# Kernel optimization log

Hardware: AMD Instinct MI355X
Metric: run time of the kernel (lower is better)

## Reference

```python
import jax, jax.numpy as jnp
import numpy as np
from jax import lax

HEADS = 4
DIM = 64
GATE_HID = 16


def setup_inputs() -> dict:
    key = jax.random.key(0)
    ks = jax.random.split(key, 12)
    b, c, h, w = 2, DIM, 48, 48
    s = 0.05
    x = jax.random.normal(ks[0], (b, c, h, w), jnp.float32)
    Wqkv = jax.random.normal(ks[1], (3 * c, c), jnp.float32) * s
    bqkv = jax.random.normal(ks[2], (3 * c,), jnp.float32) * s
    Wpos = jax.random.normal(ks[3], (3 * c, 1, 3, 3), jnp.float32) * s
    bpos = jax.random.normal(ks[4], (3 * c,), jnp.float32) * s
    Wg1 = jax.random.normal(ks[5], (GATE_HID, 1), jnp.float32) * 0.5
    bg1 = jax.random.normal(ks[6], (GATE_HID,), jnp.float32) * 0.1
    Wg2 = jax.random.normal(ks[7], (1, GATE_HID), jnp.float32) * 0.5
    bg2 = jax.random.normal(ks[8], (1,), jnp.float32) * 0.1
    Wproj = jax.random.normal(ks[9], (c, c), jnp.float32) * s
    bproj = jax.random.normal(ks[10], (c,), jnp.float32) * s
    return {"x": x, "Wqkv": Wqkv, "bqkv": bqkv, "Wpos": Wpos, "bpos": bpos,
            "Wg1": Wg1, "bg1": bg1, "Wg2": Wg2, "bg2": bg2,
            "Wproj": Wproj, "bproj": bproj}


def _forward(x, Wqkv, bqkv, Wpos, bpos, Wg1, bg1, Wg2, bg2, Wproj, bproj):
    b, c, h, w = x.shape
    n = h * w
    heads = HEADS
    hd = c // heads
    scale = hd ** -0.5
    # qkv 1x1 conv then 3x3 depthwise positional conv
    qkv = jnp.einsum('bchw,oc->bohw', x, Wqkv) + bqkv[None, :, None, None]
    qkv = lax.conv_general_dilated(
        qkv, Wpos, window_strides=(1, 1), padding='SAME',
        feature_group_count=3 * c,
        dimension_numbers=('NCHW', 'OIHW', 'NCHW')) + bpos[None, :, None, None]
    q, k, v = jnp.split(qkv, 3, axis=1)

    def to_heads(t):
        # [b,c,h,w] -> [b,heads,n,hd]
        return t.reshape(b, c, n).transpose(0, 2, 1).reshape(b, n, heads, hd).transpose(0, 2, 1, 3)

    q, k, v = to_heads(q), to_heads(k), to_heads(v)
    attn = jnp.einsum('bhid,bhjd->bhij', q, k) * scale  # [b,heads,n,n]
    prob = jax.nn.softmax(attn, axis=-1)
    entropy = -(prob * jnp.log(jnp.clip(prob, 1e-12))).sum(-1).mean(-1)  # [b,heads]
    # entropy gate: sigmoid(fc2(relu(fc1(e)))) * 0.9 + 0.1
    hgate = jax.nn.relu(entropy[..., None] @ Wg1.T + bg1)  # [b,heads,16]
    ratio = jax.nn.sigmoid(hgate @ Wg2.T + bg2)[..., 0] * 0.9 + 0.1  # [b,heads]
    # dynamic per-(batch,head) top-k along rows via rank threshold
    keep = jnp.clip(jnp.ceil(ratio * n).astype(jnp.int32), 1, n)  # [b,heads]
    sorted_desc = -jnp.sort(-attn, axis=-1)  # [b,heads,n,n]
    idx = jnp.broadcast_to((keep - 1)[:, :, None, None], (b, heads, n, 1))
    thresh = jnp.take_along_axis(sorted_desc, idx, axis=-1)  # [b,heads,n,1]
    sparse = jnp.where(attn >= thresh, attn, -jnp.inf)
    p = jax.nn.softmax(sparse, axis=-1)
    out = jnp.einsum('bhij,bhjd->bhid', p, v)  # [b,heads,n,hd]
    out = out.transpose(0, 2, 1, 3).reshape(b, n, c)
    out = out @ Wproj.T + bproj
    return out.transpose(0, 2, 1).reshape(b, c, h, w)


def reference(x, Wqkv, bqkv, Wpos, bpos, Wg1, bg1, Wg2, bg2, Wproj, bproj):
    return _forward(x, Wqkv, bqkv, Wpos, bpos, Wg1, bg1, Wg2, bg2, Wproj, bproj)
```

## Files before the change

kernel.cpp:

```cpp
#include <hip/hip_runtime.h>
#include <hip/hip_fp16.h>


#define NEG_INF (-__builtin_huge_valf())

typedef _Float16 half8_t __attribute__((ext_vector_type(8)));
typedef float floatx4 __attribute__((ext_vector_type(4)));

__device__ __forceinline__ unsigned h2key(unsigned short u) {
  return (u & 0x8000u) ? (unsigned)((~u) & 0xFFFFu) : (unsigned)(u | 0x8000u);
}
__device__ __forceinline__ float key16_to_float(unsigned k) {
  unsigned short u = (k & 0x8000u) ? (unsigned short)(k & 0x7FFFu)
                                   : (unsigned short)((~k) & 0xFFFFu);
  return __half2float(__ushort_as_half(u));
}

__device__ __forceinline__ void unpack8(uint4 v, float* o) {
  float2 f0 = __half22float2(*(__half2*)&v.x);
  float2 f1 = __half22float2(*(__half2*)&v.y);
  float2 f2 = __half22float2(*(__half2*)&v.z);
  float2 f3 = __half22float2(*(__half2*)&v.w);
  o[0] = f0.x; o[1] = f0.y; o[2] = f1.x; o[3] = f1.y;
  o[4] = f2.x; o[5] = f2.y; o[6] = f3.x; o[7] = f3.y;
}

__global__ __launch_bounds__(256) void k_dw(const float* __restrict__ x,
                                            const float* __restrict__ Wqkv,
                                            const float* __restrict__ bqkv,
                                            const float* __restrict__ Wpos,
                                            const float* __restrict__ bpos,
                                            _Float16* __restrict__ q2,
                                            _Float16* __restrict__ k2,
                                            _Float16* __restrict__ vt,
                                            float* __restrict__ ent) {
  __shared__ float smem[16][384];
  if (blockIdx.x == 0 && threadIdx.x < 8) ent[threadIdx.x] = 0.f;
  int blk = blockIdx.x;
  int chunk = blk % 9;
  int sel = (blk / 9) % 3;
  int head = (blk / 27) % 4;
  int b = blk / 108;
  int chbase = sel * 64 + head * 16;
  int bh = b * 4 + head;
  int tid = threadIdx.x;
  int p0 = chunk * 256;
  int baserow = p0 / 48;
  int rA = min(max(baserow - 1, 0), 40);

  for (int rep = 0; rep < 2; rep++) {
    int pw = tid + rep * 256;
    if (pw < 384) {
      int gpos = rA * 48 + pw;
      const float* xb = x + b * 64 * 2304 + gpos;
      float acc[16];
#pragma unroll
      for (int d = 0; d < 16; d++) acc[d] = bqkv[chbase + d];
#pragma unroll 8
      for (int c = 0; c < 64; c++) {
        float xv = xb[c * 2304];
#pragma unroll
        for (int d = 0; d < 16; d++)
          acc[d] = fmaf(Wqkv[(chbase + d) * 64 + c], xv, acc[d]);
      }
#pragma unroll
      for (int d = 0; d < 16; d++) smem[d][pw] = acc[d];
    }
  }
  __syncthreads();

  int pos = p0 + tid;
  int yy = pos / 48, xx = pos - yy * 48;
  int ry = yy - rA;
  float accv[16];
#pragma unroll
  for (int d = 0; d < 16; d++) {
    const float* w = Wpos + (chbase + d) * 9;
    float a = bpos[chbase + d];
#pragma unroll
    for (int dy = -1; dy <= 1; dy++) {
      int y2 = yy + dy;
      if ((unsigned)y2 < 48u) {
#pragma unroll
        for (int dx = -1; dx <= 1; dx++) {
          int x2 = xx + dx;
          if ((unsigned)x2 < 48u)
            a = fmaf(w[(dy + 1) * 3 + (dx + 1)], smem[d][(ry + dy) * 48 + x2],
                     a);
        }
      }
    }
    accv[d] = a;
  }

  if (sel == 2) {
#pragma unroll
    for (int d = 0; d < 16; d++)
      vt[((size_t)bh * 16 + d) * 2304 + pos] = (_Float16)accv[d];
  } else {
    _Float16 h1[16], h2[16];
#pragma unroll
    for (int d = 0; d < 16; d++) {
      float a = (sel == 0) ? accv[d] * 0.25f : accv[d];
      h1[d] = (_Float16)a;
      h2[d] = (_Float16)(a - (float)h1[d]);
    }
    _Float16* dst = ((sel == 0) ? q2 : k2) + ((size_t)bh * 2304 + pos) * 32;
    uint4* d4 = (uint4*)dst;
    d4[0] = *(uint4*)&h1[0];
    d4[1] = *(uint4*)&h1[8];
    d4[2] = *(uint4*)&h2[0];
    d4[3] = *(uint4*)&h2[8];
  }
}

template <bool STORE>
__global__ __launch_bounds__(256) void k_ent_t(const _Float16* __restrict__ q2,
                                               const _Float16* __restrict__ k2,
                                               float* __restrict__ ent,
                                               _Float16* __restrict__ lgH) {
  __shared__ __align__(16) _Float16 tBuf[4][16][72];
  __shared__ float mWv[4][16];
  __shared__ float mFin[16];
  __shared__ float sWv[4][16], uWv[4][16];

  int blk = blockIdx.x;
  int rowtile = blk % 144;
  int bh = blk / 144;
  int row0 = rowtile * 16;
  int tid = threadIdx.x, lane = tid & 63, wave = tid >> 6;
  int m16 = lane & 15, quad = lane >> 4;

  const half8_t* q2v =
      (const half8_t*)(q2 + ((size_t)bh * 2304 + row0 + m16) * 32);
  half8_t A1 = q2v[quad];
  half8_t zh = {};
  half8_t A2 = (lane < 32) ? A1 : zh;
  const half8_t* kbase = (const half8_t*)(k2 + (size_t)bh * 2304 * 32);

  float mreg[4] = {NEG_INF, NEG_INF, NEG_INF, NEG_INF};
  for (int g = 0; g < 9; g++) {
#pragma unroll
    for (int tt = 0; tt < 4; tt++) {
      int t = g * 4 + tt;
      int col = wave * 576 + t * 16 + m16;
      const half8_t* kk = kbase + (size_t)col * 4;
      half8_t b1 = kk[quad & 1];
      half8_t b2 = kk[2 + (quad & 1)];
      floatx4 acc = {};
      acc = __builtin_amdgcn_mfma_f32_16x16x32_f16(A2, b2, acc, 0, 0, 0);
      acc = __builtin_amdgcn_mfma_f32_16x16x32_f16(A1, b1, acc, 0, 0, 0);
#pragma unroll
      for (int i = 0; i < 4; i++) {
        mreg[i] = fmaxf(mreg[i], acc[i]);
        if (STORE) tBuf[wave][quad * 4 + i][tt * 16 + m16] = (_Float16)acc[i];
      }
    }
    if (STORE) {
      __syncthreads();
      int rb = lane >> 3, seg = lane & 7;
#pragma unroll
      for (int it = 0; it < 2; it++) {
        int rr = it * 8 + rb;
        uint4 vv = *(const uint4*)&tBuf[wave][rr][seg * 8];
        *(uint4*)(lgH + ((size_t)bh * 2304 + row0 + rr) * 2304 + wave * 576 +
                  g * 64 + seg * 8) = vv;
      }
      __syncthreads();
    }
  }
#pragma unroll
  for (int off = 1; off < 16; off <<= 1)
#pragma unroll
    for (int i = 0; i < 4; i++)
      mreg[i] = fmaxf(mreg[i], __shfl_xor(mreg[i], off));
  if (m16 == 0) {
#pragma unroll
    for (int i = 0; i < 4; i++) mWv[wave][quad * 4 + i] = mreg[i];
  }
  __syncthreads();
  if (tid < 16) {
    mFin[tid] = fmaxf(fmaxf(mWv[0][tid], mWv[1][tid]),
                      fmaxf(mWv[2][tid], mWv[3][tid]));
  }
  __syncthreads();

  float mrow[4];
#pragma unroll
  for (int i = 0; i < 4; i++) mrow[i] = mFin[quad * 4 + i];
  float s[4] = {0.f, 0.f, 0.f, 0.f}, u[4] = {0.f, 0.f, 0.f, 0.f};
#pragma unroll 4
  for (int t = 0; t < 36; t++) {
    int col = wave * 576 + t * 16 + m16;
    const half8_t* kk = kbase + (size_t)col * 4;
    half8_t b1 = kk[quad & 1];
    half8_t b2 = kk[2 + (quad & 1)];
    floatx4 acc = {};
    acc = __builtin_amdgcn_mfma_f32_16x16x32_f16(A2, b2, acc, 0, 0, 0);
    acc = __builtin_amdgcn_mfma_f32_16x16x32_f16(A1, b1, acc, 0, 0, 0);
#pragma unroll
    for (int i = 0; i < 4; i++) {
      float z = acc[i] - mrow[i];
      float e = __expf(z);
      s[i] += e;
      u[i] = fmaf(z, e, u[i]);
    }
  }
#pragma unroll
  for (int off = 1; off < 16; off <<= 1) {
#pragma unroll
    for (int i = 0; i < 4; i++) {
      s[i] += __shfl_xor(s[i], off);
      u[i] += __shfl_xor(u[i], off);
    }
  }
  if (m16 == 0) {
#pragma unroll
    for (int i = 0; i < 4; i++) {
      sWv[wave][quad * 4 + i] = s[i];
      uWv[wave][quad * 4 + i] = u[i];
    }
  }
  __syncthreads();
  if (tid < 16) {
    float S = sWv[0][tid] + sWv[1][tid] + sWv[2][tid] + sWv[3][tid];
    float U = uWv[0][tid] + uWv[1][tid] + uWv[2][tid] + uWv[3][tid];
    float er = __logf(S) - U / S;
    er += __shfl_xor(er, 1);
    er += __shfl_xor(er, 2);
    er += __shfl_xor(er, 4);
    er += __shfl_xor(er, 8);
    if (tid == 0) atomicAdd(&ent[bh], er);
  }
}

template <bool CACHED>
__global__ __launch_bounds__(256, 7) void k_attn_t(
    const _Float16* __restrict__ q2, const _Float16* __restrict__ k2,
    const _Float16* __restrict__ vt, const _Float16* __restrict__ lgH,
    const float* __restrict__ ent, const float* __restrict__ Wg1,
    const float* __restrict__ bg1, const float* __restrict__ Wg2,
    const float* __restrict__ bg2, float* __restrict__ oh) {
  __shared__ __align__(16) _Float16 pbuf[4][2320];
  __shared__ float sS[4];
  __shared__ float mShF[4][4];
  __shared__ __align__(16) float redSh[4][64];

  int a = blockIdx.x;
  int v8 = a & 7;
  int idx = a >> 3;
  int q = idx & 3;
  int pi = idx >> 2;
  int bh = pi / 18;
  int rowtile = v8 + (pi % 18) * 8;
  int rowblk = rowtile * 4 + q;
  int row0 = rowblk * 4;
  int tid = threadIdx.x, lane = tid & 63, wave = tid >> 6;

  float eAvg = ent[bh] * (1.f / 2304.f);
  float gacc = bg2[0];
#pragma unroll
  for (int i = 0; i < 16; i++) {
    float h = fmaxf(fmaf(eAvg, Wg1[i], bg1[i]), 0.f);
    gacc = fmaf(h, Wg2[i], gacc);
  }
  float ratio = 0.9f / (1.f + __expf(-gacc)) + 0.1f;
  int kp = (int)ceilf(ratio * 2304.f);
  unsigned keep = (unsigned)min(max(kp, 1), 2304);

  float v[36];
  float m;
  if (CACHED) {
    const _Float16* src = lgH + ((size_t)bh * 2304 + row0 + wave) * 2304;
    const uint4* s4 = (const uint4*)src;
    float mx = NEG_INF;
#pragma unroll
    for (int it = 0; it < 4; it++) {
      uint4 r = s4[lane + it * 64];
      unpack8(r, &v[it * 8]);
    }
    {
      uint2 r2 = *(const uint2*)(src + 2048 + lane * 4);
      float2 f0 = __half22float2(*(__half2*)&r2.x);
      float2 f1 = __half22float2(*(__half2*)&r2.y);
      v[32] = f0.x; v[33] = f0.y; v[34] = f1.x; v[35] = f1.y;
    }
#pragma unroll
    for (int i = 0; i < 36; i++) mx = fmaxf(mx, v[i]);
#pragma unroll
    for (int off = 1; off < 64; off <<= 1) mx = fmaxf(mx, __shfl_xor(mx, off));
    m = mx;
  } else {
    int m16 = lane & 15, quad = lane >> 4;
    const half8_t* q2v =
        (const half8_t*)(q2 + ((size_t)bh * 2304 + row0 + (m16 & 3)) * 32);
    half8_t A1 = q2v[quad];
    half8_t zh = {};
    half8_t A2 = (lane < 32) ? A1 : zh;
    const half8_t* kbase = (const half8_t*)(k2 + (size_t)bh * 2304 * 32);
    float ml[4] = {NEG_INF, NEG_INF, NEG_INF, NEG_INF};
#pragma unroll 4
    for (int t = 0; t < 36; t++) {
      int ct = wave * 36 + t;
      int col = ct * 16 + m16;
      const half8_t* kk = kbase + (size_t)col * 4;
      half8_t b1 = kk[quad & 1];
      half8_t b2 = kk[2 + (quad & 1)];
      floatx4 acc = {};
      acc = __builtin_amdgcn_mfma_f32_16x16x32_f16(A2, b2, acc, 0, 0, 0);
      acc = __builtin_amdgcn_mfma_f32_16x16x32_f16(A1, b1, acc, 0, 0, 0);
      if (lane < 16) {
#pragma unroll
        for (int i = 0; i < 4; i++) {
          pbuf[i][ct * 16 + lane] = (_Float16)acc[i];
          ml[i] = fmaxf(ml[i], acc[i]);
        }
      }
    }
#pragma unroll
    for (int off = 1; off < 16; off <<= 1)
#pragma unroll
      for (int i = 0; i < 4; i++) ml[i] = fmaxf(ml[i], __shfl_xor(ml[i], off));
    if (lane == 0) {
#pragma unroll
      for (int i = 0; i < 4; i++) mShF[wave][i] = ml[i];
    }
    __syncthreads();
    m = fmaxf(fmaxf(mShF[0][wave], mShF[1][wave]),
              fmaxf(mShF[2][wave], mShF[3][wave]));
    const _Float16* src = pbuf[wave];
    const uint4* s4 = (const uint4*)src;
#pragma unroll
    for (int it = 0; it < 4; it++) unpack8(s4[lane + it * 64], &v[it * 8]);
    uint2 r2 = *(const uint2*)(src + 2048 + lane * 4);
    float2 f0 = __half22float2(*(__half2*)&r2.x);
    float2 f1 = __half22float2(*(__half2*)&r2.y);
    v[32] = f0.x; v[33] = f0.y; v[34] = f1.x; v[35] = f1.y;
  }

  float th;
  {
    unsigned T = 0u;
    for (int bit = 15; bit >= 0; --bit) {
      unsigned cand = T | (1u << bit);
      float cf = key16_to_float(cand);
      unsigned cnt = 0u;
#pragma unroll
      for (int i = 0; i < 36; i++)
        cnt += (unsigned)__popcll(__ballot(v[i] >= cf));
      if (cnt >= keep) {
        T = cand;
        if (cnt == keep) break;
      }
    }
    th = key16_to_float(T);
  }

  {
    float sp = 0.f;
    uint4* prow4 = (uint4*)pbuf[wave];
#pragma unroll
    for (int it = 0; it < 4; it++) {
      float p[8];
#pragma unroll
      for (int e = 0; e < 8; e++) {
        float av = v[it * 8 + e];
        p[e] = (av >= th) ? __expf(av - m) : 0.f;
        sp += p[e];
      }
      uint4 o;
      __half2 h0 = __floats2half2_rn(p[0], p[1]); o.x = *(unsigned*)&h0;
      __half2 h1 = __floats2half2_rn(p[2], p[3]); o.y = *(unsigned*)&h1;
      __half2 h2 = __floats2half2_rn(p[4], p[5]); o.z = *(unsigned*)&h2;
      __half2 h3 = __floats2half2_rn(p[6], p[7]); o.w = *(unsigned*)&h3;
      prow4[lane + it * 64] = o;
    }
    {
      float p0 = (v[32] >= th) ? __expf(v[32] - m) : 0.f;
      float p1 = (v[33] >= th) ? __expf(v[33] - m) : 0.f;
      float p2 = (v[34] >= th) ? __expf(v[34] - m) : 0.f;
      float p3 = (v[35] >= th) ? __expf(v[35] - m) : 0.f;
      sp += (p0 + p1) + (p2 + p3);
      uint2 o;
      __half2 h0 = __floats2half2_rn(p0, p1); o.x = *(unsigned*)&h0;
      __half2 h1 = __floats2half2_rn(p2, p3); o.y = *(unsigned*)&h1;
      *(uint2*)(pbuf[wave] + 2048 + lane * 4) = o;
    }
#pragma unroll
    for (int off = 1; off < 64; off <<= 1) sp += __shfl_xor(sp, off);
    if (lane == 0) sS[wave] = sp;
  }
  __syncthreads();

  {
    int m16 = lane & 15, quad = lane >> 4;
    const _Float16* vrow = vt + ((size_t)bh * 16 + m16) * 2304;
    const _Float16* prow = pbuf[m16 & 3];
    int jb0 = wave * 576 + quad * 8;
    floatx4 acc = {};
#pragma unroll 6
    for (int t = 0; t < 18; t++) {
      int jb = jb0 + t * 32;
      half8_t a2 = *(const half8_t*)&prow[jb];
      half8_t b2 = *(const half8_t*)&vrow[jb];
      acc = __builtin_amdgcn_mfma_f32_16x16x32_f16(a2, b2, acc, 0, 0, 0);
    }
    if (lane < 16) {
      *(floatx4*)&redSh[wave][m16 * 4] = acc;
    }
  }
  __syncthreads();
  if (tid < 64) {
    int r = tid & 3, d = tid >> 2;
    float s2 = redSh[0][d * 4 + r] + redSh[1][d * 4 + r] +
               redSh[2][d * 4 + r] + redSh[3][d * 4 + r];
    oh[((size_t)(bh * 2304 + row0 + r)) * 16 + d] = s2 / sS[r];
  }
}

__global__ __launch_bounds__(256) void k_proj(const float* __restrict__ oh,
                                              const float* __restrict__ Wp,
                                              const float* __restrict__ bp,
                                              float* __restrict__ out) {
  int blk = blockIdx.x;
  int chunk = blk % 9;
  int cog = (blk / 9) % 16;
  int b = blk / (9 * 16);
  int co0 = cog * 4;
  int pos = chunk * 256 + threadIdx.x;
  float a0 = bp[co0 + 0], a1 = bp[co0 + 1], a2 = bp[co0 + 2], a3 = bp[co0 + 3];
#pragma unroll
  for (int head = 0; head < 4; head++) {
    const float4* op =
        (const float4*)(oh + ((size_t)((b * 4 + head) * 2304 + pos)) * 16);
#pragma unroll
    for (int p = 0; p < 4; p++) {
      float4 o4 = op[p];
#pragma unroll
      for (int i = 0; i < 4; i++) {
        const float* wr = Wp + (co0 + i) * 64 + head * 16 + p * 4;
        float* ai = (i == 0) ? &a0 : ((i == 1) ? &a1 : ((i == 2) ? &a2 : &a3));
        *ai = fmaf(wr[0], o4.x, *ai);
        *ai = fmaf(wr[1], o4.y, *ai);
        *ai = fmaf(wr[2], o4.z, *ai);
        *ai = fmaf(wr[3], o4.w, *ai);
      }
    }
  }
  out[(b * 64 + co0 + 0) * 2304 + pos] = a0;
  out[(b * 64 + co0 + 1) * 2304 + pos] = a1;
  out[(b * 64 + co0 + 2) * 2304 + pos] = a2;
  out[(b * 64 + co0 + 3) * 2304 + pos] = a3;
}

extern "C" void kernel_launch(void* const* d_in, const int* in_sizes, int n_in,
                              void* d_out, int out_size, void* d_ws,
                              size_t ws_size, hipStream_t stream) {
  const float* x    = (const float*)d_in[0];
  const float* Wqkv = (const float*)d_in[1];
  const float* bqkv = (const float*)d_in[2];
  const float* Wpos = (const float*)d_in[3];
  const float* bpos = (const float*)d_in[4];
  const float* Wg1  = (const float*)d_in[5];
  const float* bg1  = (const float*)d_in[6];
  const float* Wg2  = (const float*)d_in[7];
  const float* bg2  = (const float*)d_in[8];
  const float* Wpr  = (const float*)d_in[9];
  const float* bpr  = (const float*)d_in[10];
  float* out = (float*)d_out;

  const size_t lgBytes = (size_t)8 * 2304 * 2304 * 2;
  const size_t baseBytes =
      (size_t)(294912 + 8) * 4 + (size_t)(2 * 589824 + 294912) * 2;
  bool cached = ws_size >= lgBytes + baseBytes;

  char* base = (char*)d_ws;
  _Float16* lgH = nullptr;
  if (cached) {
    lgH = (_Float16*)base;
    base += lgBytes;
  }
  float* oh = (float*)base;
  float* ent = oh + 294912;
  _Float16* q2 = (_Float16*)(ent + 8);
  _Float16* k2 = q2 + 589824;
  _Float16* vt = k2 + 589824;

  hipLaunchKernelGGL(k_dw, dim3(216), dim3(256), 0, stream,
                     x, Wqkv, bqkv, Wpos, bpos, q2, k2, vt, ent);
  if (cached) {
    hipLaunchKernelGGL((k_ent_t<true>), dim3(8 * 144), dim3(256), 0, stream,
                       q2, k2, ent, lgH);
    hipLaunchKernelGGL((k_attn_t<true>), dim3(8 * 576), dim3(256), 0, stream,
                       q2, k2, vt, lgH, ent, Wg1, bg1, Wg2, bg2, oh);
  } else {
    hipLaunchKernelGGL((k_ent_t<false>), dim3(8 * 144), dim3(256), 0, stream,
                       q2, k2, ent, lgH);
    hipLaunchKernelGGL((k_attn_t<false>), dim3(8 * 576), dim3(256), 0, stream,
                       q2, k2, vt, lgH, ent, Wg1, bg1, Wg2, bg2, oh);
  }
  hipLaunchKernelGGL(k_proj, dim3(2 * 16 * 9), dim3(256), 0, stream,
                     oh, Wpr, bpr, out);
}
```

Before: 218.3 us.

## Split QKV 1x1 conv into its own high-parallelism kernel before depthwise conv

Moves the 1x1 QKV projection out of the depthwise-conv kernel into a separate kernel launched on 864 blocks, each computing 4 output channels for 256 positions, and writes fp32 results to a new workspace buffer. The depthwise kernel then loads its halo tile from that buffer instead of recomputing the projection for 384 halo positions per block. This removes redundant halo recomputation and the low-occupancy 216-block projection, at the cost of an extra launch and a round trip of about 3.5 MB through global memory. The workspace requirement grows, which may change whether the cached-logits path is enabled.

```diff
diff --git a/kernel.cpp b/kernel.cpp
--- a/kernel.cpp
+++ b/kernel.cpp
@@ -7,9 +7,6 @@
 typedef _Float16 half8_t __attribute__((ext_vector_type(8)));
 typedef float floatx4 __attribute__((ext_vector_type(4)));
 
-__device__ __forceinline__ unsigned h2key(unsigned short u) {
-  return (u & 0x8000u) ? (unsigned)((~u) & 0xFFFFu) : (unsigned)(u | 0x8000u);
-}
 __device__ __forceinline__ float key16_to_float(unsigned k) {
   unsigned short u = (k & 0x8000u) ? (unsigned short)(k & 0x7FFFu)
                                    : (unsigned short)((~k) & 0xFFFFu);
@@ -25,17 +22,46 @@
   o[4] = f2.x; o[5] = f2.y; o[6] = f3.x; o[7] = f3.y;
 }
 
-__global__ __launch_bounds__(256) void k_dw(const float* __restrict__ x,
-                                            const float* __restrict__ Wqkv,
-                                            const float* __restrict__ bqkv,
+__global__ __launch_bounds__(256) void k_qkv(const float* __restrict__ x,
+                                             const float* __restrict__ W,
+                                             const float* __restrict__ bias,
+                                             float* __restrict__ out,
+                                             float* __restrict__ ent) {
+  if (blockIdx.x == 0 && threadIdx.x < 8) ent[threadIdx.x] = 0.f;
+  int blk = blockIdx.x;
+  int chunk = blk % 9;
+  int og = (blk / 9) % 48;
+  int b = blk / (9 * 48);
+  int o0 = og * 4;
+  int pos = chunk * 256 + threadIdx.x;
+  const float* xb = x + b * 64 * 2304 + pos;
+  const float* w0 = W + (o0 + 0) * 64;
+  const float* w1 = W + (o0 + 1) * 64;
+  const float* w2 = W + (o0 + 2) * 64;
+  const float* w3 = W + (o0 + 3) * 64;
+  float a0 = bias[o0 + 0], a1 = bias[o0 + 1];
+  float a2 = bias[o0 + 2], a3 = bias[o0 + 3];
+#pragma unroll
+  for (int c = 0; c < 64; c++) {
+    float xv = xb[c * 2304];
+    a0 = fmaf(w0[c], xv, a0);
+    a1 = fmaf(w1[c], xv, a1);
+    a2 = fmaf(w2[c], xv, a2);
+    a3 = fmaf(w3[c], xv, a3);
+  }
+  out[(b * 192 + o0 + 0) * 2304 + pos] = a0;
+  out[(b * 192 + o0 + 1) * 2304 + pos] = a1;
+  out[(b * 192 + o0 + 2) * 2304 + pos] = a2;
+  out[(b * 192 + o0 + 3) * 2304 + pos] = a3;
+}
+
+__global__ __launch_bounds__(256) void k_dw(const float* __restrict__ qkv,
                                             const float* __restrict__ Wpos,
                                             const float* __restrict__ bpos,
                                             _Float16* __restrict__ q2,
                                             _Float16* __restrict__ k2,
-                                            _Float16* __restrict__ vt,
-                                            float* __restrict__ ent) {
+                                            _Float16* __restrict__ vt) {
   __shared__ float smem[16][384];
-  if (blockIdx.x == 0 && threadIdx.x < 8) ent[threadIdx.x] = 0.f;
   int blk = blockIdx.x;
   int chunk = blk % 9;
   int sel = (blk / 9) % 3;
@@ -48,24 +74,15 @@
   int baserow = p0 / 48;
   int rA = min(max(baserow - 1, 0), 40);
 
-  for (int rep = 0; rep < 2; rep++) {
-    int pw = tid + rep * 256;
-    if (pw < 384) {
-      int gpos = rA * 48 + pw;
-      const float* xb = x + b * 64 * 2304 + gpos;
-      float acc[16];
-#pragma unroll
-      for (int d = 0; d < 16; d++) acc[d] = bqkv[chbase + d];
-#pragma unroll 8
-      for (int c = 0; c < 64; c++) {
-        float xv = xb[c * 2304];
-#pragma unroll
-        for (int d = 0; d < 16; d++)
-          acc[d] = fmaf(Wqkv[(chbase + d) * 64 + c], xv, acc[d]);
-      }
-#pragma unroll
-      for (int d = 0; d < 16; d++) smem[d][pw] = acc[d];
-    }
+  const float* src = qkv + (size_t)(b * 192 + chbase) * 2304;
+#pragma unroll
+  for (int l = 0; l < 24; l++) {
+    int idx = tid + l * 256;
+    int ch = idx / 384;
+    int off = idx - ch * 384;
+    int rr = off / 48;
+    int cc = off - rr * 48;
+    smem[ch][off] = src[(size_t)ch * 2304 + (rA + rr) * 48 + cc];
   }
   __syncthreads();
 
@@ -470,8 +487,8 @@
   float* out = (float*)d_out;
 
   const size_t lgBytes = (size_t)8 * 2304 * 2304 * 2;
-  const size_t baseBytes =
-      (size_t)(294912 + 8) * 4 + (size_t)(2 * 589824 + 294912) * 2;
+  const size_t baseBytes = (size_t)(884736 + 294912 + 8) * 4 +
+                           (size_t)(2 * 589824 + 294912) * 2;
   bool cached = ws_size >= lgBytes + baseBytes;
 
   char* base = (char*)d_ws;
@@ -480,14 +497,17 @@
     lgH = (_Float16*)base;
     base += lgBytes;
   }
-  float* oh = (float*)base;
+  float* qkv_raw = (float*)base;
+  float* oh = qkv_raw + 884736;
   float* ent = oh + 294912;
   _Float16* q2 = (_Float16*)(ent + 8);
   _Float16* k2 = q2 + 589824;
   _Float16* vt = k2 + 589824;
 
+  hipLaunchKernelGGL(k_qkv, dim3(2 * 48 * 9), dim3(256), 0, stream,
+                     x, Wqkv, bqkv, qkv_raw, ent);
   hipLaunchKernelGGL(k_dw, dim3(216), dim3(256), 0, stream,
-                     x, Wqkv, bqkv, Wpos, bpos, q2, k2, vt, ent);
+                     qkv_raw, Wpos, bpos, q2, k2, vt);
   if (cached) {
     hipLaunchKernelGGL((k_ent_t<true>), dim3(8 * 144), dim3(256), 0, stream,
                        q2, k2, ent, lgH);
```

Result: faster. 203.9 us (-6.6%).
